# Kernel tuning notes

Measured on AMD Instinct MI355X. Metric: run time of the kernel, lower is better.

## Reference

```python
import jax, jax.numpy as jnp
import numpy as np

B, N = 2, 256
RC = 6.0
BOX = 12.0
# (center_radius, eta) for G2; kappas for G3; (eta, zeta, lambda) for G4/G5
G2_PARAMS = [(rs, eta) for rs in (0.0, 2.0) for eta in (0.1, 1.0)]
G3_KAPPAS = [1.0, 2.0]
G45_PARAMS = [(eta, zeta, lam) for eta in (0.01, 0.1) for zeta in (1.0, 4.0) for lam in (-1.0, 1.0)]


def _fc(r, rc):
    # Behler cosine cutoff: 0.5*(cos(pi r / rc) + 1) for r < rc, else 0
    return 0.5 * (jnp.cos(jnp.pi * r / rc) + 1.0) * (r < rc)


def setup_inputs() -> dict:
    key = jax.random.key(0)
    k1, k2 = jax.random.split(key)
    atomic_numbers = jax.random.randint(k1, (N,), 1, 10).astype(jnp.float32)
    coordinates = jax.random.uniform(k2, (B, N, 3), dtype=jnp.float32) * BOX
    return {"atomic_numbers": atomic_numbers, "coordinates": coordinates}


def reference(atomic_numbers, coordinates):
    b, n, _ = coordinates.shape
    # r_ij vector = x_i - x_j, matching coords.unsqueeze(-2) - coords.unsqueeze(-3)
    dvec = coordinates[:, :, None, :] - coordinates[:, None, :, :]        # [B,N,N,3]
    sq = jnp.sum(dvec * dvec, axis=-1)                                    # [B,N,N]
    pair_mask = ~jnp.eye(n, dtype=bool)                                   # j != i
    sq_safe = jnp.where(pair_mask, sq, 1.0)
    r = jnp.where(pair_mask, jnp.sqrt(sq_safe), 0.0)                      # [B,N,N]
    fcr = _fc(r, RC) * pair_mask                                          # cutoff, self excluded

    feats = [jnp.broadcast_to(atomic_numbers, (b, n))]
    # G1: sum_j fc(r_ij)
    feats.append(jnp.sum(fcr, axis=-1))
    # G2: sum_j exp(-eta*(r_ij - Rs)^2) * fc(r_ij)
    for rs, eta in G2_PARAMS:
        feats.append(jnp.sum(jnp.exp(-eta * (r - rs) ** 2) * fcr, axis=-1))
    # G3: sum_j cos(kappa * r_ij) * fc(r_ij)
    for kappa in G3_KAPPAS:
        feats.append(jnp.sum(jnp.cos(kappa * r) * fcr, axis=-1))

    # shared angular (triplet) quantities, each [B,N,N,N]
    dot = jnp.einsum('bijc,bikc->bijk', dvec, dvec)
    denom = r[:, :, :, None] * r[:, :, None, :]
    cos_t = dot / jnp.where(denom > 0, denom, 1.0)
    sq_ij = sq[:, :, :, None]
    sq_ik = sq[:, :, None, :]
    sq_jk = sq[:, None, :, :]
    sq3 = sq_ij + sq_ik + sq_jk
    sq2 = sq_ij + sq_ik
    # fc products: fcr already zero on the diagonal, so fc3 vanishes whenever
    # j==i, k==i, or j==k (full triplet mask for G4)
    fc3 = fcr[:, :, :, None] * fcr[:, :, None, :] * fcr[:, None, :, :]
    fc2 = fcr[:, :, :, None] * fcr[:, :, None, :] * pair_mask[None, None, :, :]

    # G4: 2^(1-zeta) sum_{j!=k} (1+lam*cos)^zeta exp(-eta*(rij^2+rik^2+rjk^2)) fc fc fc
    for eta, zeta, lam in G45_PARAMS:
        ang = jnp.maximum(1.0 + lam * cos_t, 0.0) ** zeta
        feats.append((2.0 ** (1.0 - zeta)) * jnp.sum(ang * jnp.exp(-eta * sq3) * fc3, axis=(-2, -1)))
    # G5: 2^(1-zeta) sum_{j!=k} (1+lam*cos)^zeta exp(-eta*(rij^2+rik^2)) fc fc
    for eta, zeta, lam in G45_PARAMS:
        ang = jnp.maximum(1.0 + lam * cos_t, 0.0) ** zeta
        feats.append((2.0 ** (1.0 - zeta)) * jnp.sum(ang * jnp.exp(-eta * sq2) * fc2, axis=(-2, -1)))

    return jnp.stack(feats, axis=-1)  # [B, N, 24]
```

## Files before the change

kernel.cpp:

```cpp
#include <hip/hip_runtime.h>
#include <math.h>

#define NN 256
#define NF 24
#define RCUT 6.0f
#define PI_F 3.14159265358979323846f
#define NSEG 16

#define GEO_OFF  (4096)
#define WGT_OFF  (4096 + 2*1024*1024)
#define PART_OFF (4096 + 4*1024*1024)

__global__ __launch_bounds__(64) void setup_kernel(
    const float* __restrict__ Z,
    const float* __restrict__ coords,
    float* __restrict__ out,
    void* __restrict__ wsv)
{
    const int i = blockIdx.x, b = blockIdx.y, lane = threadIdx.x;
    const int ai = b * NN + i;
    int* m_arr = (int*)wsv;
    float4* geoC = (float4*)((char*)wsv + GEO_OFF) + (size_t)ai * NN;
    float4* wgtC = (float4*)((char*)wsv + WGT_OFF) + (size_t)ai * NN;

    const float* cb = coords + (size_t)b * NN * 3;
    const float xi = cb[i * 3 + 0], yi = cb[i * 3 + 1], zi = cb[i * 3 + 2];

    float acc[7];
#pragma unroll
    for (int t = 0; t < 7; t++) acc[t] = 0.0f;

    int m = 0;
#pragma unroll
    for (int rnd = 0; rnd < 4; ++rnd) {
        const int j = lane + (rnd << 6);
        const float xj = cb[j * 3 + 0], yj = cb[j * 3 + 1], zj = cb[j * 3 + 2];
        const float dx = xi - xj, dy = yi - yj, dz = zi - zj;
        const float r2 = dx * dx + dy * dy + dz * dz;
        const float r  = sqrtf(r2);
        const bool incut = (j != i) && (r < RCUT);
        const float fc = incut ? 0.5f * (__cosf((PI_F / RCUT) * r) + 1.0f) : 0.0f;
        acc[0] += fc;
        acc[1] += __expf(-0.1f * r2) * fc;
        acc[2] += __expf(-1.0f * r2) * fc;
        const float d = r - 2.0f;
        acc[3] += __expf(-0.1f * d * d) * fc;
        acc[4] += __expf(-1.0f * d * d) * fc;
        acc[5] += __cosf(r) * fc;
        acc[6] += __cosf(2.0f * r) * fc;
        const unsigned long long bal = __ballot(incut);
        if (incut) {
            const int p = m + __popcll(bal & ((1ULL << lane) - 1ULL));
            geoC[p] = make_float4(dx, dy, dz, 1.0f / r);
            wgtC[p] = make_float4(fc, __expf(-0.01f * r2), __expf(-0.1f * r2), 0.0f);
        }
        m += __popcll(bal);
    }
    if (lane == 0) m_arr[ai] = m;

#pragma unroll
    for (int t = 0; t < 7; t++) {
        float v = acc[t];
        for (int off = 32; off > 0; off >>= 1) v += __shfl_down(v, off, 64);
        acc[t] = v;
    }
    if (lane == 0) {
        float* ob = out + (size_t)ai * NF;
        ob[0] = Z[i];
#pragma unroll
        for (int t = 0; t < 7; t++) ob[1 + t] = acc[t];
    }
}

__global__ __launch_bounds__(256) void pair_kernel(
    const void* __restrict__ wsv_in, void* __restrict__ wsv_out)
{
    const int i = blockIdx.x, b = blockIdx.y;
    const int tid = threadIdx.x, lane = tid & 63, wave = tid >> 6;
    const int seg = blockIdx.z * 4 + wave;
    const int ai = b * NN + i;

    const int* m_arr = (const int*)wsv_in;
    const float4* geoC = (const float4*)((const char*)wsv_in + GEO_OFF) + (size_t)ai * NN;
    const float4* wgtC = (const float4*)((const char*)wsv_in + WGT_OFF) + (size_t)ai * NN;
    float* part = (float*)((char*)wsv_out + PART_OFF);

    __shared__ float4 geo[NN];
    __shared__ float4 wgt[NN];
    __shared__ float red[4][16];

    const int m = m_arr[ai];
    for (int idx = tid; idx < m; idx += 256) {
        geo[idx] = geoC[idx];
        wgt[idx] = wgtC[idx];
    }
    __syncthreads();

    float acc[16];
#pragma unroll
    for (int t = 0; t < 16; t++) acc[t] = 0.0f;

    if (m >= 2) {
        const int Rfull = (m - 1) >> 1;
        const int tlo = 1 + (Rfull * seg) / NSEG;
        const int thi = (Rfull * (seg + 1)) / NSEG;
        const bool halfseg = (seg == NSEG - 1) && ((m & 1) == 0);
        const int mh = m >> 1;
        for (int rnd = 0; rnd < 4; ++rnd) {
            const int jj = lane + (rnd << 6);
            if (jj >= m) break;
            const float4 gj = geo[jj];
            const float4 wj = wgt[jj];
            for (int t = tlo; t <= thi + (halfseg && jj < mh ? 1 : 0); ++t) {
                int kk = jj + ((t > thi) ? mh : t); if (kk >= m) kk -= m;
                const float4 g = geo[kk];
                const float4 w = wgt[kk];
                const float ddx = gj.x - g.x, ddy = gj.y - g.y, ddz = gj.z - g.z;
                const float sqjk = ddx * ddx + ddy * ddy + ddz * ddz;
                const float rjk = sqrtf(sqjk);
                const float fcjk = (rjk < RCUT) ? 0.5f * (__cosf((PI_F / RCUT) * rjk) + 1.0f) : 0.0f;
                const float dot = gj.x * g.x + gj.y * g.y + gj.z * g.z;
                const float cost = dot * gj.w * g.w;
                const float base = wj.x * w.x;
                const float f3 = base * fcjk;
                const float e2a = wj.y * w.y;
                const float e2b = wj.z * w.z;
                const float e3a = e2a * __expf(-0.01f * sqjk);
                const float e3b = e2b * __expf(-0.1f * sqjk);
                const float c1m = fmaxf(1.0f - cost, 0.0f);
                const float c1p = fmaxf(1.0f + cost, 0.0f);
                const float c2m = c1m * c1m, c2p = c1p * c1p;
                const float c4m = c2m * c2m, c4p = c2p * c2p;
                const float w3a = e3a * f3, w3b = e3b * f3;
                const float w2a = e2a * base, w2b = e2b * base;
                acc[0]  += c1m * w3a;  acc[1]  += c1p * w3a;
                acc[2]  += c4m * w3a;  acc[3]  += c4p * w3a;
                acc[4]  += c1m * w3b;  acc[5]  += c1p * w3b;
                acc[6]  += c4m * w3b;  acc[7]  += c4p * w3b;
                acc[8]  += c1m * w2a;  acc[9]  += c1p * w2a;
                acc[10] += c4m * w2a;  acc[11] += c4p * w2a;
                acc[12] += c1m * w2b;  acc[13] += c1p * w2b;
                acc[14] += c4m * w2b;  acc[15] += c4p * w2b;
            }
        }
    }

#pragma unroll
    for (int t = 0; t < 16; t++) {
        float v = acc[t];
        for (int off = 32; off > 0; off >>= 1) v += __shfl_down(v, off, 64);
        if (lane == 0) red[wave][t] = v;
    }
    __syncthreads();
    if (tid < 64) {
        const int w2 = tid >> 4, f = tid & 15;
        part[((size_t)ai * NSEG + (blockIdx.z * 4 + w2)) * 16 + f] = red[w2][f];
    }
}

__global__ __launch_bounds__(256) void reduce_kernel(
    const void* __restrict__ wsv, float* __restrict__ out)
{
    const int idx = blockIdx.x * 256 + threadIdx.x;
    const int f  = idx & 15;
    const int ai = idx >> 4;
    const float* p = (const float*)((const char*)wsv + PART_OFF)
                   + ((size_t)ai * NSEG) * 16 + f;
    float v = 0.0f;
#pragma unroll
    for (int s = 0; s < NSEG; ++s) v += p[s * 16];
    v *= ((f & 3) >= 2) ? 0.25f : 2.0f;
    out[(size_t)ai * NF + 8 + f] = v;
}

extern "C" void kernel_launch(void* const* d_in, const int* in_sizes, int n_in,
                              void* d_out, int out_size, void* d_ws, size_t ws_size,
                              hipStream_t stream) {
    const float* Z = (const float*)d_in[0];
    const float* coords = (const float*)d_in[1];
    float* out = (float*)d_out;
    setup_kernel<<<dim3(NN, 2), dim3(64), 0, stream>>>(Z, coords, out, d_ws);
    pair_kernel<<<dim3(NN, 2, NSEG / 4), dim3(256), 0, stream>>>(d_ws, d_ws);
    reduce_kernel<<<dim3(2 * NN * 16 / 256), dim3(256), 0, stream>>>(d_ws, out);
}
```

Measured before the change: 75.16 us.

## Fuse setup, pair and reduce kernels into one per-atom kernel

Merges the three kernels into a single 512-thread block per atom. The block builds the compacted neighbor list straight into shared memory and does the full triplet sum with 8 wave segments, then writes the final features itself. This removes two launches, the workspace round trip for the neighbor arrays and partials, and the separate reduction pass. In exchange the grid shrinks from 2048 blocks of 256 threads to 512 blocks of 512 threads, so there may be less parallelism to hide latency and more per-wave load imbalance.

```diff
diff --git a/kernel.cpp b/kernel.cpp
--- a/kernel.cpp
+++ b/kernel.cpp
@@ -5,94 +5,64 @@
 #define NF 24
 #define RCUT 6.0f
 #define PI_F 3.14159265358979323846f
-#define NSEG 16
+#define NSEG 8
 
-#define GEO_OFF  (4096)
-#define WGT_OFF  (4096 + 2*1024*1024)
-#define PART_OFF (4096 + 4*1024*1024)
-
-__global__ __launch_bounds__(64) void setup_kernel(
+__global__ __launch_bounds__(512, 4) void feat_kernel(
     const float* __restrict__ Z,
     const float* __restrict__ coords,
-    float* __restrict__ out,
-    void* __restrict__ wsv)
+    float* __restrict__ out)
 {
-    const int i = blockIdx.x, b = blockIdx.y, lane = threadIdx.x;
-    const int ai = b * NN + i;
-    int* m_arr = (int*)wsv;
-    float4* geoC = (float4*)((char*)wsv + GEO_OFF) + (size_t)ai * NN;
-    float4* wgtC = (float4*)((char*)wsv + WGT_OFF) + (size_t)ai * NN;
+    const int i = blockIdx.x, b = blockIdx.y;
+    const int tid = threadIdx.x, lane = tid & 63, wave = tid >> 6;
+
+    __shared__ float4 geo[NN];
+    __shared__ float4 wgt[NN];
+    __shared__ int   wave_cnt[4];
+    __shared__ float rad[4][7];
+    __shared__ float red[8][16];
 
     const float* cb = coords + (size_t)b * NN * 3;
     const float xi = cb[i * 3 + 0], yi = cb[i * 3 + 1], zi = cb[i * 3 + 2];
 
-    float acc[7];
+    float dx = 0, dy = 0, dz = 0, r2 = 0, r = 0, fc = 0;
+    bool incut = false;
+    if (tid < NN) {
+        const float xj = cb[tid * 3 + 0], yj = cb[tid * 3 + 1], zj = cb[tid * 3 + 2];
+        dx = xi - xj; dy = yi - yj; dz = zi - zj;
+        r2 = dx * dx + dy * dy + dz * dz;
+        r  = sqrtf(r2);
+        incut = (tid != i) && (r < RCUT);
+        fc = incut ? 0.5f * (__cosf((PI_F / RCUT) * r) + 1.0f) : 0.0f;
+
+        float racc[7];
+        racc[0] = fc;
+        racc[1] = __expf(-0.1f * r2) * fc;
+        racc[2] = __expf(-1.0f * r2) * fc;
+        const float d = r - 2.0f;
+        racc[3] = __expf(-0.1f * d * d) * fc;
+        racc[4] = __expf(-1.0f * d * d) * fc;
+        racc[5] = __cosf(r) * fc;
+        racc[6] = __cosf(2.0f * r) * fc;
 #pragma unroll
-    for (int t = 0; t < 7; t++) acc[t] = 0.0f;
+        for (int t = 0; t < 7; t++) {
+            float v = racc[t];
+            for (int off = 32; off > 0; off >>= 1) v += __shfl_down(v, off, 64);
+            if (lane == 0) rad[wave][t] = v;
+        }
+        const unsigned long long bal = __ballot(incut);
+        if (lane == 0) wave_cnt[wave] = __popcll(bal);
+    }
+    __syncthreads();
 
-    int m = 0;
+    const int m = wave_cnt[0] + wave_cnt[1] + wave_cnt[2] + wave_cnt[3];
+    if (tid < NN && incut) {
+        const unsigned long long bal = __ballot(incut);
+        int base = 0;
 #pragma unroll
-    for (int rnd = 0; rnd < 4; ++rnd) {
-        const int j = lane + (rnd << 6);
-        const float xj = cb[j * 3 + 0], yj = cb[j * 3 + 1], zj = cb[j * 3 + 2];
-        const float dx = xi - xj, dy = yi - yj, dz = zi - zj;
-        const float r2 = dx * dx + dy * dy + dz * dz;
-        const float r  = sqrtf(r2);
-        const bool incut = (j != i) && (r < RCUT);
-        const float fc = incut ? 0.5f * (__cosf((PI_F / RCUT) * r) + 1.0f) : 0.0f;
-        acc[0] += fc;
-        acc[1] += __expf(-0.1f * r2) * fc;
-        acc[2] += __expf(-1.0f * r2) * fc;
-        const float d = r - 2.0f;
-        acc[3] += __expf(-0.1f * d * d) * fc;
-        acc[4] += __expf(-1.0f * d * d) * fc;
-        acc[5] += __cosf(r) * fc;
-        acc[6] += __cosf(2.0f * r) * fc;
-        const unsigned long long bal = __ballot(incut);
-        if (incut) {
-            const int p = m + __popcll(bal & ((1ULL << lane) - 1ULL));
-            geoC[p] = make_float4(dx, dy, dz, 1.0f / r);
-            wgtC[p] = make_float4(fc, __expf(-0.01f * r2), __expf(-0.1f * r2), 0.0f);
-        }
-        m += __popcll(bal);
-    }
-    if (lane == 0) m_arr[ai] = m;
-
-#pragma unroll
-    for (int t = 0; t < 7; t++) {
-        float v = acc[t];
-        for (int off = 32; off > 0; off >>= 1) v += __shfl_down(v, off, 64);
-        acc[t] = v;
-    }
-    if (lane == 0) {
-        float* ob = out + (size_t)ai * NF;
-        ob[0] = Z[i];
-#pragma unroll
-        for (int t = 0; t < 7; t++) ob[1 + t] = acc[t];
-    }
-}
-
-__global__ __launch_bounds__(256) void pair_kernel(
-    const void* __restrict__ wsv_in, void* __restrict__ wsv_out)
-{
-    const int i = blockIdx.x, b = blockIdx.y;
-    const int tid = threadIdx.x, lane = tid & 63, wave = tid >> 6;
-    const int seg = blockIdx.z * 4 + wave;
-    const int ai = b * NN + i;
-
-    const int* m_arr = (const int*)wsv_in;
-    const float4* geoC = (const float4*)((const char*)wsv_in + GEO_OFF) + (size_t)ai * NN;
-    const float4* wgtC = (const float4*)((const char*)wsv_in + WGT_OFF) + (size_t)ai * NN;
-    float* part = (float*)((char*)wsv_out + PART_OFF);
-
-    __shared__ float4 geo[NN];
-    __shared__ float4 wgt[NN];
-    __shared__ float red[4][16];
-
-    const int m = m_arr[ai];
-    for (int idx = tid; idx < m; idx += 256) {
-        geo[idx] = geoC[idx];
-        wgt[idx] = wgtC[idx];
+        for (int w = 0; w < 4; w++) if (w < wave) base += wave_cnt[w];
+        const int p = base + __popcll(bal & ((1ULL << lane) - 1ULL));
+        geo[p] = make_float4(dx, dy, dz, 1.0f / r);
+        wgt[p] = make_float4(fc, __expf(-0.01f * r2), __expf(-0.1f * r2), 0.0f);
     }
     __syncthreads();
 
@@ -102,16 +72,17 @@
 
     if (m >= 2) {
         const int Rfull = (m - 1) >> 1;
-        const int tlo = 1 + (Rfull * seg) / NSEG;
-        const int thi = (Rfull * (seg + 1)) / NSEG;
-        const bool halfseg = (seg == NSEG - 1) && ((m & 1) == 0);
+        const int tlo = 1 + (Rfull * wave) / NSEG;
+        const int thi = (Rfull * (wave + 1)) / NSEG;
+        const bool halfseg = (wave == NSEG - 1) && ((m & 1) == 0);
         const int mh = m >> 1;
         for (int rnd = 0; rnd < 4; ++rnd) {
             const int jj = lane + (rnd << 6);
             if (jj >= m) break;
             const float4 gj = geo[jj];
             const float4 wj = wgt[jj];
-            for (int t = tlo; t <= thi + (halfseg && jj < mh ? 1 : 0); ++t) {
+            const int tend = thi + ((halfseg && jj < mh) ? 1 : 0);
+            for (int t = tlo; t <= tend; ++t) {
                 int kk = jj + ((t > thi) ? mh : t); if (kk >= m) kk -= m;
                 const float4 g = geo[kk];
                 const float4 w = wgt[kk];
@@ -121,8 +92,8 @@
                 const float fcjk = (rjk < RCUT) ? 0.5f * (__cosf((PI_F / RCUT) * rjk) + 1.0f) : 0.0f;
                 const float dot = gj.x * g.x + gj.y * g.y + gj.z * g.z;
                 const float cost = dot * gj.w * g.w;
-                const float base = wj.x * w.x;
-                const float f3 = base * fcjk;
+                const float base2 = wj.x * w.x;
+                const float f3 = base2 * fcjk;
                 const float e2a = wj.y * w.y;
                 const float e2b = wj.z * w.z;
                 const float e3a = e2a * __expf(-0.01f * sqjk);
@@ -132,7 +103,7 @@
                 const float c2m = c1m * c1m, c2p = c1p * c1p;
                 const float c4m = c2m * c2m, c4p = c2p * c2p;
                 const float w3a = e3a * f3, w3b = e3b * f3;
-                const float w2a = e2a * base, w2b = e2b * base;
+                const float w2a = e2a * base2, w2b = e2b * base2;
                 acc[0]  += c1m * w3a;  acc[1]  += c1p * w3a;
                 acc[2]  += c4m * w3a;  acc[3]  += c4p * w3a;
                 acc[4]  += c1m * w3b;  acc[5]  += c1p * w3b;
@@ -152,25 +123,20 @@
         if (lane == 0) red[wave][t] = v;
     }
     __syncthreads();
-    if (tid < 64) {
-        const int w2 = tid >> 4, f = tid & 15;
-        part[((size_t)ai * NSEG + (blockIdx.z * 4 + w2)) * 16 + f] = red[w2][f];
+
+    float* ob = out + ((size_t)b * NN + i) * NF;
+    if (tid < 16) {
+        float v = 0.0f;
+#pragma unroll
+        for (int w = 0; w < 8; w++) v += red[w][tid];
+        v *= ((tid & 3) >= 2) ? 0.25f : 2.0f;
+        ob[8 + tid] = v;
+    } else if (tid >= 32 && tid < 39) {
+        const int t = tid - 32;
+        ob[1 + t] = rad[0][t] + rad[1][t] + rad[2][t] + rad[3][t];
+    } else if (tid == 39) {
+        ob[0] = Z[i];
     }
-}
-
-__global__ __launch_bounds__(256) void reduce_kernel(
-    const void* __restrict__ wsv, float* __restrict__ out)
-{
-    const int idx = blockIdx.x * 256 + threadIdx.x;
-    const int f  = idx & 15;
-    const int ai = idx >> 4;
-    const float* p = (const float*)((const char*)wsv + PART_OFF)
-                   + ((size_t)ai * NSEG) * 16 + f;
-    float v = 0.0f;
-#pragma unroll
-    for (int s = 0; s < NSEG; ++s) v += p[s * 16];
-    v *= ((f & 3) >= 2) ? 0.25f : 2.0f;
-    out[(size_t)ai * NF + 8 + f] = v;
 }
 
 extern "C" void kernel_launch(void* const* d_in, const int* in_sizes, int n_in,
@@ -179,7 +145,5 @@
     const float* Z = (const float*)d_in[0];
     const float* coords = (const float*)d_in[1];
     float* out = (float*)d_out;
-    setup_kernel<<<dim3(NN, 2), dim3(64), 0, stream>>>(Z, coords, out, d_ws);
-    pair_kernel<<<dim3(NN, 2, NSEG / 4), dim3(256), 0, stream>>>(d_ws, d_ws);
-    reduce_kernel<<<dim3(2 * NN * 16 / 256), dim3(256), 0, stream>>>(d_ws, out);
+    feat_kernel<<<dim3(NN, 2), dim3(512), 0, stream>>>(Z, coords, out);
 }
```

Result: faster. 67.96 us (-9.6%).
